# Optimization experiments

Hardware: AMD Instinct MI355X
Metric: run time of the kernel (lower is better)

Reference implementation:

```python
import jax, jax.numpy as jnp
import numpy as np
import math

N = 50000   # nodes
E = 800000  # edges
D = 128     # in/out dim
T = 4       # node types
H = 8       # heads (forced: Linear(8,64).view(-1, H, 8))
DK = D // H
HD = 8      # h_mat feature dim


def setup_inputs() -> dict:
    key = jax.random.key(0)
    ks = jax.random.split(key, 16)
    g = lambda k, shp, fan: jax.random.uniform(k, shp, jnp.float32, -1.0, 1.0) * math.sqrt(6.0 / fan)
    return {
        "meta_xs": jax.random.normal(ks[0], (N, D), jnp.float32),
        "node_type": jax.random.randint(ks[1], (N,), 0, T),
        "edge_index": jax.random.randint(ks[2], (2, E), 0, N),
        "h_mat": jax.random.normal(ks[3], (N, HD), jnp.float32),
        "sub_W": g(ks[4], (T, D, D), 2 * D),
        "sub_b": jnp.zeros((T, D), jnp.float32),
        "neigh_W": g(ks[5], (T, D, D), 2 * D),
        "neigh_b": jnp.zeros((T, D), jnp.float32),
        "hsub_W": g(ks[6], (HD, H * HD), HD + H * HD),
        "hsub_b": jnp.zeros((H * HD,), jnp.float32),
        "hneigh_W": g(ks[7], (HD, H * HD), HD + H * HD),
        "hneigh_b": jnp.zeros((H * HD,), jnp.float32),
        "relation_att": g(ks[8], (T, H, DK), H + DK),
        "relation_h_att": g(ks[9], (T, H, HD), H + HD),
        "ln_gamma": jnp.ones((D,), jnp.float32),
        "ln_beta": jnp.zeros((D,), jnp.float32),
    }


def _hgt_forward(meta_xs, h_mat, sub_W, sub_b, neigh_W, neigh_b, hsub_W, hsub_b,
                 hneigh_W, hneigh_b, relation_att, relation_h_att, ln_gamma, ln_beta,
                 node_type, edge_index):
    n = meta_xs.shape[0]
    e = edge_index.shape[1]
    src = edge_index[0]  # edge_index_j (neighbor)
    dst = edge_index[1]  # edge_index_i (sub / target)
    sqrt_dk = math.sqrt(DK)
    d_h = math.sqrt(H)

    # per-node, type-selected linear projections (sub by own type, neigh by own type)
    q_all = jnp.einsum('nd,tdo->tno', meta_xs, sub_W) + sub_b[:, None, :]      # [T,N,D]
    k_all = jnp.einsum('nd,tdo->tno', meta_xs, neigh_W) + neigh_b[:, None, :]  # [T,N,D]
    ar = jnp.arange(n)
    q_node = q_all[node_type, ar]  # [N,D] sub_linear[type_i](x_i)
    k_node = k_all[node_type, ar]  # [N,D] neigh_linear[type_j](x_j)

    h_sub_node = (h_mat @ hsub_W + hsub_b).reshape(n, H, HD)
    h_neigh_node = (h_mat @ hneigh_W + hneigh_b).reshape(n, H, HD)

    st = node_type[dst]  # sub type per edge selects relation params
    h_s = h_sub_node[dst]    # [E,H,8]
    h_n = h_neigh_node[src]  # [E,H,8]
    att_h = jnp.sum(jnp.tanh(h_s * h_n) * relation_h_att[st], axis=-1) / d_h  # [E,H]

    q_e = q_node[dst].reshape(e, H, DK)
    k_e = k_node[src].reshape(e, H, DK)
    att = jnp.sum(jnp.tanh(q_e * k_e) * relation_att[st], axis=-1) / sqrt_dk * att_h  # [E,H]

    # edge softmax over destination segments
    m = jax.ops.segment_max(att, dst, num_segments=n)  # [N,H]
    ea = jnp.exp(att - m[dst])
    denom = jax.ops.segment_sum(ea, dst, num_segments=n)
    alpha = ea / (denom[dst] + 1e-16)  # [E,H]

    msg = (k_e * alpha[:, :, None]).reshape(e, D)
    aggr = jax.ops.segment_sum(msg, dst, num_segments=n)  # [N,D]

    out = jax.nn.gelu(aggr, approximate=False)
    mu = jnp.mean(out, axis=-1, keepdims=True)
    var = jnp.var(out, axis=-1, keepdims=True)
    return (out - mu) * jax.lax.rsqrt(var + 1e-5) * ln_gamma + ln_beta


def reference(meta_xs, node_type, edge_index, h_mat, sub_W, sub_b, neigh_W, neigh_b,
              hsub_W, hsub_b, hneigh_W, hneigh_b, relation_att, relation_h_att,
              ln_gamma, ln_beta):
    return _hgt_forward(meta_xs, h_mat, sub_W, sub_b, neigh_W, neigh_b, hsub_W, hsub_b,
                        hneigh_W, hneigh_b, relation_att, relation_h_att, ln_gamma, ln_beta,
                        node_type, edge_index)
```

## Files before the change

kernel.cpp:

```cpp
#include <hip/hip_runtime.h>

typedef __bf16 bf16x8 __attribute__((ext_vector_type(8)));
typedef float f32x4 __attribute__((ext_vector_type(4)));

__device__ __forceinline__ float exp2_fast(float x){
#if __has_builtin(__builtin_amdgcn_exp2f)
  return __builtin_amdgcn_exp2f(x);
#else
  return __expf(x * 0.69314718055994531f);
#endif
}
template<int CTRL>
__device__ __forceinline__ float dpp_add(float x){
  union { float f; int i; } a, b;
  a.f = x;
  b.i = __builtin_amdgcn_mov_dpp(a.i, CTRL, 0xF, 0xF, true);
  return x + b.f;
}
__device__ __forceinline__ float sum4(float x){
  x = dpp_add<0xB1>(x);
  x = dpp_add<0x4E>(x);
  return x;
}
__device__ __forceinline__ unsigned int cvt_pk_bf16(float lo, float hi){
  unsigned int r;
  asm("v_cvt_pk_bf16_f32 %0, %1, %2" : "=v"(r) : "v"(lo), "v"(hi));
  return r;
}
__device__ __forceinline__ unsigned short f2bf1(float f){
  return (unsigned short)cvt_pk_bf16(f, f);
}
__device__ __forceinline__ bf16x8 ld_bf8(const unsigned short* p){
  union { uint4 u; bf16x8 v; } c;
  c.u = *reinterpret_cast<const uint4*>(p);
  return c.v;
}
__device__ __forceinline__ bf16x8 ld_f32_to_bf8(const float* p){
  float4 lo = *reinterpret_cast<const float4*>(p);
  float4 hi = *reinterpret_cast<const float4*>(p + 4);
  union { unsigned int u[4]; bf16x8 v; } c;
  c.u[0] = cvt_pk_bf16(lo.x, lo.y);
  c.u[1] = cvt_pk_bf16(lo.z, lo.w);
  c.u[2] = cvt_pk_bf16(hi.x, hi.y);
  c.u[3] = cvt_pk_bf16(hi.z, hi.w);
  return c.v;
}

__global__ void k_ll_h_w(const int* ei, int* cursor, unsigned short* bucket, int E,
                         const int* ntype, int* tcur, int* nbt, int Npad, int N,
                         const float* h_mat, const float* hsW, const float* hsb,
                         const float* hnW, const float* hnb,
                         float2* hs2, char* hnc, int LB, int NB, int HB,
                         const float* subW, const float* neighW,
                         unsigned short* wts, unsigned short* wtn){
  int b = blockIdx.x;
  if (b < LB){
    int i = b*256 + threadIdx.x;
    if (i >= E) return;
    int d = ei[E + i];
    int s = ei[i];
    int pos = atomicAdd(&cursor[d << 4], 1);
    if (pos < 128) bucket[(size_t)d*128 + pos] = (unsigned short)s;
  } else if (b < LB + NB){
    int i = (b - LB)*256 + threadIdx.x;
    if (i >= N) return;
    int lane = threadIdx.x & 63;
    int myt = ntype[i];
    unsigned long long below = (lane == 0) ? 0ull : ((~0ull) >> (64 - lane));
    #pragma unroll
    for (int tt = 0; tt < 4; ++tt){
      unsigned long long mask = __ballot(myt == tt);
      if (mask){
        int leader = __ffsll((long long)mask) - 1;
        int base = 0;
        if (lane == leader) base = atomicAdd(&tcur[tt], __popcll(mask));
        base = __shfl(base, leader);
        if (myt == tt){
          int pos = base + __popcll(mask & below);
          nbt[tt*Npad + pos] = i;
        }
      }
    }
  } else if (b < LB + NB + HB){
    int i = (b - LB - NB)*256 + threadIdx.x;
    if (i >= N*32) return;
    int n = i >> 5, l = i & 31;
    const float* hm = h_mat + (size_t)n*8;
    const float2* hsW2 = reinterpret_cast<const float2*>(hsW);
    const float2* hnW2 = reinterpret_cast<const float2*>(hnW);
    float s0=0.f, s1=0.f, n0=0.f, n1=0.f;
    #pragma unroll
    for (int d = 0; d < 8; ++d){
      float hv = hm[d];
      float2 ws2 = hsW2[d*32 + l];
      float2 wn2 = hnW2[d*32 + l];
      s0 += hv * ws2.x; s1 += hv * ws2.y;
      n0 += hv * wn2.x; n1 += hv * wn2.y;
    }
    float2 bs = reinterpret_cast<const float2*>(hsb)[l];
    float2 bn = reinterpret_cast<const float2*>(hnb)[l];
    hs2[(size_t)i] = make_float2(s0 + bs.x, s1 + bs.y);
    *reinterpret_cast<unsigned int*>(hnc + (size_t)n*128 + l*4)
        = cvt_pk_bf16(n0 + bn.x, n1 + bn.y);
  } else {
    int i = (b - LB - NB - HB)*256 + threadIdx.x;
    int w = i >> 16;
    int r = i & 65535;
    int t = r >> 14;
    int rem = r & 16383;
    int o = rem >> 7;
    int kd = rem & 127;
    const float* src = w ? neighW : subW;
    unsigned short* dstp = w ? wtn : wts;
    dstp[(t << 14) + (o << 7) + kd] = f2bf1(src[(t << 14) + (kd << 7) + o]);
  }
}

__global__ __launch_bounds__(256) void k_qk_mfma(const float* X,
      const unsigned short* wts, const unsigned short* wtn,
      const float* sub_b, const float* neigh_b,
      const int* nbt, const int* tcur, int Npad,
      float* q, char* kkc){
  int b = blockIdx.x;
  int t = -1, chunk = 0, acc = 0;
  #pragma unroll
  for (int tt = 0; tt < 4; ++tt){
    int cnt = tcur[tt];
    int nc = (cnt + 63) >> 6;
    if (t < 0 && b < acc + nc){ t = tt; chunk = b - acc; }
    acc += nc;
  }
  if (t < 0) return;
  int lane = threadIdx.x & 63;
  int w = threadIdx.x >> 6;
  int quad = lane >> 4, l16 = lane & 15;
  int cnt = tcur[t];
  int p = chunk*64 + w*16 + l16;
  bool ok = p < cnt;
  int nid = nbt[t*Npad + (ok ? p : 0)];
  bf16x8 xb[4];
  #pragma unroll
  for (int kk = 0; kk < 4; ++kk)
    xb[kk] = ld_f32_to_bf8(X + (size_t)nid*128 + kk*32 + quad*8);
  #pragma unroll
  for (int pj = 0; pj < 2; ++pj){
    const unsigned short* Wt = pj ? wtn : wts;
    const float* bias = pj ? neigh_b : sub_b;
    #pragma unroll
    for (int ot = 0; ot < 8; ++ot){
      f32x4 c = {0.f, 0.f, 0.f, 0.f};
      #pragma unroll
      for (int kk = 0; kk < 4; ++kk){
        bf16x8 wa = ld_bf8(Wt + ((size_t)t << 14) + ((size_t)(ot*16 + l16) << 7)
                              + kk*32 + quad*8);
        c = __builtin_amdgcn_mfma_f32_16x16x32_bf16(wa, xb[kk], c, 0, 0, 0);
      }
      int o0 = ot*16 + quad*4;
      float4 b4 = *reinterpret_cast<const float4*>(bias + t*128 + o0);
      if (ok){
        if (pj == 0){
          float4 v = make_float4(c[0]+b4.x, c[1]+b4.y, c[2]+b4.z, c[3]+b4.w);
          *reinterpret_cast<float4*>(q + (size_t)nid*128 + o0) = v;
        } else {
          uint2 pk;
          pk.x = cvt_pk_bf16(c[0]+b4.x, c[1]+b4.y);
          pk.y = cvt_pk_bf16(c[2]+b4.z, c[3]+b4.w);
          *reinterpret_cast<uint2*>(kkc + ((size_t)nid << 8) + (size_t)(o0 << 1)) = pk;
        }
      }
    }
  }
}

__global__ __launch_bounds__(256) void k_edge(const float* q, const char* kkc,
      const char* hnc, const float2* hs2, const int* cursor,
      const unsigned short* bucket, const int* ntype,
      const float* rel_att, const float* rel_h_att,
      const float* ln_g, const float* ln_b,
      float* out, int N){
  int wid = (blockIdx.x*blockDim.x + threadIdx.x) >> 6;
  if (wid >= N) return;
  int lane = threadIdx.x & 63;
  int l = lane & 31;
  int half = (lane >> 5) & 1;
  int t4 = l & 3, head = l >> 2;
  const float TLOG2E = 2.8853900817779268f;
  float4 qv = *reinterpret_cast<const float4*>(q + (size_t)wid*128 + l*4);
  float qe0 = qv.x*TLOG2E, qe1 = qv.y*TLOG2E, qe2 = qv.z*TLOG2E, qe3 = qv.w*TLOG2E;
  float2 hv = hs2[(size_t)wid*32 + l];
  float he0 = hv.x*TLOG2E, he1 = hv.y*TLOG2E;
  int st = ntype[wid];
  int rb = st*8 + head;
  float4 ra = *reinterpret_cast<const float4*>(rel_att + rb*16 + t4*4);
  float2 rh = *reinterpret_cast<const float2*>(rel_h_att + rb*8 + t4*2);
  float c0 = -0.5f*ra.x, c1 = -0.5f*ra.y, c2 = -0.5f*ra.z, c3 = -0.5f*ra.w;
  float cs = 0.25f*(ra.x + ra.y + ra.z + ra.w);
  const float HSC = 0.35355339059327373f * 1.4426950408889634f;
  float rh0 = rh.x*HSC, rh1 = rh.y*HSC;
  float ch0 = -2.f*rh0, ch1 = -2.f*rh1, chs = rh0 + rh1;
  float s = 0.f, a0 = 0.f, a1 = 0.f, a2 = 0.f, a3 = 0.f;

  int deg = __builtin_amdgcn_readfirstlane(cursor[wid << 4]);
  if (deg > 128) deg = 128;
  unsigned bkt = reinterpret_cast<const unsigned*>(bucket)[(size_t)wid*64 + lane];
  int niter = (deg + 1) >> 1;
  const char* kk_l = kkc + l*8;
  const char* hn_l = hnc + l*4;

  struct KH { uint2 k; unsigned h; };
  auto lp = [&](int g)->KH {
    int gg = g < niter ? g : 0;
    unsigned v = (unsigned)__builtin_amdgcn_readlane((int)bkt, gg);
    int sA = (int)(v & 0xffffu);
    int sB = (2*gg + 1 < deg) ? (int)(v >> 16) : sA;
    int sy = half ? sB : sA;
    KH r;
    r.k = *reinterpret_cast<const uint2*>(kk_l + ((size_t)(unsigned)sy << 8));
    r.h = *reinterpret_cast<const unsigned*>(hn_l + ((size_t)(unsigned)sy << 7));
    return r;
  };
  auto pr = [&](KH P, int g){
    union { unsigned u; float f; } k0,k1,k2,k3,h0,h1;
    k0.u = P.k.x << 16; k1.u = P.k.x & 0xffff0000u;
    k2.u = P.k.y << 16; k3.u = P.k.y & 0xffff0000u;
    h0.u = P.h << 16;   h1.u = P.h & 0xffff0000u;
    float e0 = exp2_fast(qe0*k0.f), e1 = exp2_fast(qe1*k1.f);
    float e2 = exp2_fast(qe2*k2.f), e3 = exp2_fast(qe3*k3.f);
    float f0 = exp2_fast(he0*h0.f), f1 = exp2_fast(he1*h1.f);
    float r0 = __builtin_amdgcn_rcpf(e0 + 1.f), r1 = __builtin_amdgcn_rcpf(e1 + 1.f);
    float r2 = __builtin_amdgcn_rcpf(e2 + 1.f), r3 = __builtin_amdgcn_rcpf(e3 + 1.f);
    float g0 = __builtin_amdgcn_rcpf(f0 + 1.f), g1 = __builtin_amdgcn_rcpf(f1 + 1.f);
    float pp = fmaf(c0,r0, fmaf(c1,r1, fmaf(c2,r2, fmaf(c3,r3, cs))));
    float ph = fmaf(ch0,g0, fmaf(ch1,g1, chs));
    pp = sum4(pp);
    ph = sum4(ph);
    float w = exp2_fast(pp * ph);
    w = (2*g + half < deg) ? w : 0.f;
    s += w;
    a0 = fmaf(w, k0.f, a0); a1 = fmaf(w, k1.f, a1);
    a2 = fmaf(w, k2.f, a2); a3 = fmaf(w, k3.f, a3);
  };

  if (niter > 0){
    KH A = lp(0);
    KH B = lp(1);
    for (int g = 0; g < niter; g += 2){
      KH C = lp(g+2);
      pr(A, g);
      KH D = lp(g+3);
      if (g+1 < niter) pr(B, g+1);
      A = C; B = D;
    }
  }
  s  += __shfl_xor(s, 32);
  a0 += __shfl_xor(a0, 32); a1 += __shfl_xor(a1, 32);
  a2 += __shfl_xor(a2, 32); a3 += __shfl_xor(a3, 32);

  float inv = 1.0f / (s + 1e-16f);
  float x0 = a0*inv, x1 = a1*inv, x2 = a2*inv, x3 = a3*inv;
  const float IS2 = 0.70710678118654752f;
  x0 = 0.5f*x0*(1.f + erff(x0*IS2));
  x1 = 0.5f*x1*(1.f + erff(x1*IS2));
  x2 = 0.5f*x2*(1.f + erff(x2*IS2));
  x3 = 0.5f*x3*(1.f + erff(x3*IS2));
  float sm = x0+x1+x2+x3;
  float sq = x0*x0 + x1*x1 + x2*x2 + x3*x3;
  #pragma unroll
  for (int d = 1; d < 32; d <<= 1){ sm += __shfl_xor(sm, d); sq += __shfl_xor(sq, d); }
  float mu = sm * (1.f/128.f);
  float var = fmaxf(sq * (1.f/128.f) - mu*mu, 0.f);
  float r = rsqrtf(var + 1e-5f);
  if (half == 0){
    float4 g4 = *reinterpret_cast<const float4*>(ln_g + l*4);
    float4 b4 = *reinterpret_cast<const float4*>(ln_b + l*4);
    float4 o4 = make_float4((x0-mu)*r*g4.x + b4.x, (x1-mu)*r*g4.y + b4.y,
                            (x2-mu)*r*g4.z + b4.z, (x3-mu)*r*g4.w + b4.w);
    *reinterpret_cast<float4*>(out + (size_t)wid*128 + l*4) = o4;
  }
}

extern "C" void kernel_launch(void* const* d_in, const int* in_sizes, int n_in,
                              void* d_out, int out_size, void* d_ws, size_t ws_size,
                              hipStream_t stream) {
  const float* meta_xs  = (const float*)d_in[0];
  const int*   node_type= (const int*)d_in[1];
  const int*   edge_idx = (const int*)d_in[2];
  const float* h_mat    = (const float*)d_in[3];
  const float* sub_W    = (const float*)d_in[4];
  const float* sub_b    = (const float*)d_in[5];
  const float* neigh_W  = (const float*)d_in[6];
  const float* neigh_b  = (const float*)d_in[7];
  const float* hsub_W   = (const float*)d_in[8];
  const float* hsub_b   = (const float*)d_in[9];
  const float* hneigh_W = (const float*)d_in[10];
  const float* hneigh_b = (const float*)d_in[11];
  const float* rel_att  = (const float*)d_in[12];
  const float* rel_hatt = (const float*)d_in[13];
  const float* ln_g     = (const float*)d_in[14];
  const float* ln_b     = (const float*)d_in[15];

  const int N = in_sizes[0] / 128;
  const int E = in_sizes[2] / 2;
  const int Npad = (N + 63) & ~63;

  char* wbase = (char*)d_ws;
  size_t o = 0;
  auto carve = [&](size_t bytes)->char* {
    char* p = wbase + o;
    o = (o + bytes + 255) & ~(size_t)255;
    return p;
  };
  float*          q      = (float*)carve((size_t)N*128*4);
  char*           kkc    = carve((size_t)N*256);
  char*           hnc    = carve((size_t)N*128);
  float2*         hs2    = (float2*)carve((size_t)N*32*8);
  unsigned short* bucket = (unsigned short*)carve((size_t)N*128*2);
  int*            cursor = (int*)carve((size_t)N*16*4);
  int*            tmeta  = (int*)carve(64);
  int*            nbt    = (int*)carve((size_t)4*Npad*4);
  unsigned short* wts    = (unsigned short*)carve((size_t)4*128*128*2);
  unsigned short* wtn    = (unsigned short*)carve((size_t)4*128*128*2);
  if (o > ws_size) return;

  int* tcur = tmeta;

  const int LB = (E + 255) / 256;
  const int NB = (N + 255) / 256;
  const int HB = (N*32 + 255) / 256;
  const int WB = (2*4*128*128) / 256;

  hipMemsetAsync(cursor, 0, (size_t)N*64 + 64, stream);
  k_ll_h_w  <<<LB + NB + HB + WB, 256, 0, stream>>>(edge_idx, cursor, bucket, E,
                                               node_type, tcur, nbt, Npad, N,
                                               h_mat, hsub_W, hsub_b, hneigh_W, hneigh_b,
                                               hs2, hnc, LB, NB, HB,
                                               sub_W, neigh_W, wts, wtn);
  k_qk_mfma <<<((N+63)>>6)+4, 256, 0, stream>>>(meta_xs, wts, wtn, sub_b, neigh_b,
                                                nbt, tcur, Npad, q, kkc);
  k_edge    <<<(N+3)/4, 256, 0, stream>>>(q, kkc, hnc, hs2, cursor, bucket, node_type,
                                          rel_att, rel_hatt, ln_g, ln_b,
                                          (float*)d_out, N);
}
```

Measured before the change: 290.4 us.

## Co-schedule edge bucketing and h-projection with MFMA QK projection kernel

Regroups work across the prep kernels. The first kernel now only does type-sorting of nodes and weight transpose. The edge bucketing (atomics) and h_mat projections move into the same launch as the MFMA Q/K projection, so the latency-bound atomic scatter overlaps with compute. Edge bucketing also becomes a grid-stride loop with 512 blocks that issues four independent atomics per thread to raise memory-level parallelism. The risk is contention and imbalance between block roles in the mixed kernel.

```diff
diff --git a/kernel.cpp b/kernel.cpp
--- a/kernel.cpp
+++ b/kernel.cpp
@@ -46,23 +46,12 @@
   return c.v;
 }
 
-__global__ void k_ll_h_w(const int* ei, int* cursor, unsigned short* bucket, int E,
-                         const int* ntype, int* tcur, int* nbt, int Npad, int N,
-                         const float* h_mat, const float* hsW, const float* hsb,
-                         const float* hnW, const float* hnb,
-                         float2* hs2, char* hnc, int LB, int NB, int HB,
-                         const float* subW, const float* neighW,
-                         unsigned short* wts, unsigned short* wtn){
+__global__ void k_prep(const int* ntype, int* tcur, int* nbt, int Npad, int N,
+                       const float* subW, const float* neighW,
+                       unsigned short* wts, unsigned short* wtn, int NB){
   int b = blockIdx.x;
-  if (b < LB){
+  if (b < NB){
     int i = b*256 + threadIdx.x;
-    if (i >= E) return;
-    int d = ei[E + i];
-    int s = ei[i];
-    int pos = atomicAdd(&cursor[d << 4], 1);
-    if (pos < 128) bucket[(size_t)d*128 + pos] = (unsigned short)s;
-  } else if (b < LB + NB){
-    int i = (b - LB)*256 + threadIdx.x;
     if (i >= N) return;
     int lane = threadIdx.x & 63;
     int myt = ntype[i];
@@ -81,29 +70,8 @@
         }
       }
     }
-  } else if (b < LB + NB + HB){
-    int i = (b - LB - NB)*256 + threadIdx.x;
-    if (i >= N*32) return;
-    int n = i >> 5, l = i & 31;
-    const float* hm = h_mat + (size_t)n*8;
-    const float2* hsW2 = reinterpret_cast<const float2*>(hsW);
-    const float2* hnW2 = reinterpret_cast<const float2*>(hnW);
-    float s0=0.f, s1=0.f, n0=0.f, n1=0.f;
-    #pragma unroll
-    for (int d = 0; d < 8; ++d){
-      float hv = hm[d];
-      float2 ws2 = hsW2[d*32 + l];
-      float2 wn2 = hnW2[d*32 + l];
-      s0 += hv * ws2.x; s1 += hv * ws2.y;
-      n0 += hv * wn2.x; n1 += hv * wn2.y;
-    }
-    float2 bs = reinterpret_cast<const float2*>(hsb)[l];
-    float2 bn = reinterpret_cast<const float2*>(hnb)[l];
-    hs2[(size_t)i] = make_float2(s0 + bs.x, s1 + bs.y);
-    *reinterpret_cast<unsigned int*>(hnc + (size_t)n*128 + l*4)
-        = cvt_pk_bf16(n0 + bn.x, n1 + bn.y);
   } else {
-    int i = (b - LB - NB - HB)*256 + threadIdx.x;
+    int i = (b - NB)*256 + threadIdx.x;
     int w = i >> 16;
     int r = i & 65535;
     int t = r >> 14;
@@ -116,59 +84,108 @@
   }
 }
 
-__global__ __launch_bounds__(256) void k_qk_mfma(const float* X,
+__global__ __launch_bounds__(256) void k_mix(const float* X,
       const unsigned short* wts, const unsigned short* wtn,
       const float* sub_b, const float* neigh_b,
       const int* nbt, const int* tcur, int Npad,
-      float* q, char* kkc){
+      float* q, char* kkc,
+      const int* ei, int* cursor, unsigned short* bucket, int E,
+      const float* h_mat, const float* hsW, const float* hsb,
+      const float* hnW, const float* hnb,
+      float2* hs2, char* hnc, int N, int MB, int SB){
   int b = blockIdx.x;
-  int t = -1, chunk = 0, acc = 0;
-  #pragma unroll
-  for (int tt = 0; tt < 4; ++tt){
-    int cnt = tcur[tt];
-    int nc = (cnt + 63) >> 6;
-    if (t < 0 && b < acc + nc){ t = tt; chunk = b - acc; }
-    acc += nc;
-  }
-  if (t < 0) return;
-  int lane = threadIdx.x & 63;
-  int w = threadIdx.x >> 6;
-  int quad = lane >> 4, l16 = lane & 15;
-  int cnt = tcur[t];
-  int p = chunk*64 + w*16 + l16;
-  bool ok = p < cnt;
-  int nid = nbt[t*Npad + (ok ? p : 0)];
-  bf16x8 xb[4];
-  #pragma unroll
-  for (int kk = 0; kk < 4; ++kk)
-    xb[kk] = ld_f32_to_bf8(X + (size_t)nid*128 + kk*32 + quad*8);
-  #pragma unroll
-  for (int pj = 0; pj < 2; ++pj){
-    const unsigned short* Wt = pj ? wtn : wts;
-    const float* bias = pj ? neigh_b : sub_b;
-    #pragma unroll
-    for (int ot = 0; ot < 8; ++ot){
-      f32x4 c = {0.f, 0.f, 0.f, 0.f};
+  if (b < MB){
+    int t = -1, chunk = 0, acc = 0;
+    #pragma unroll
+    for (int tt = 0; tt < 4; ++tt){
+      int cnt = tcur[tt];
+      int nc = (cnt + 63) >> 6;
+      if (t < 0 && b < acc + nc){ t = tt; chunk = b - acc; }
+      acc += nc;
+    }
+    if (t < 0) return;
+    int lane = threadIdx.x & 63;
+    int w = threadIdx.x >> 6;
+    int quad = lane >> 4, l16 = lane & 15;
+    int cnt = tcur[t];
+    int p = chunk*64 + w*16 + l16;
+    bool ok = p < cnt;
+    int nid = nbt[t*Npad + (ok ? p : 0)];
+    bf16x8 xb[4];
+    #pragma unroll
+    for (int kk = 0; kk < 4; ++kk)
+      xb[kk] = ld_f32_to_bf8(X + (size_t)nid*128 + kk*32 + quad*8);
+    #pragma unroll
+    for (int pj = 0; pj < 2; ++pj){
+      const unsigned short* Wt = pj ? wtn : wts;
+      const float* bias = pj ? neigh_b : sub_b;
       #pragma unroll
-      for (int kk = 0; kk < 4; ++kk){
-        bf16x8 wa = ld_bf8(Wt + ((size_t)t << 14) + ((size_t)(ot*16 + l16) << 7)
-                              + kk*32 + quad*8);
-        c = __builtin_amdgcn_mfma_f32_16x16x32_bf16(wa, xb[kk], c, 0, 0, 0);
-      }
-      int o0 = ot*16 + quad*4;
-      float4 b4 = *reinterpret_cast<const float4*>(bias + t*128 + o0);
-      if (ok){
-        if (pj == 0){
-          float4 v = make_float4(c[0]+b4.x, c[1]+b4.y, c[2]+b4.z, c[3]+b4.w);
-          *reinterpret_cast<float4*>(q + (size_t)nid*128 + o0) = v;
-        } else {
-          uint2 pk;
-          pk.x = cvt_pk_bf16(c[0]+b4.x, c[1]+b4.y);
-          pk.y = cvt_pk_bf16(c[2]+b4.z, c[3]+b4.w);
-          *reinterpret_cast<uint2*>(kkc + ((size_t)nid << 8) + (size_t)(o0 << 1)) = pk;
+      for (int ot = 0; ot < 8; ++ot){
+        f32x4 c = {0.f, 0.f, 0.f, 0.f};
+        #pragma unroll
+        for (int kk = 0; kk < 4; ++kk){
+          bf16x8 wa = ld_bf8(Wt + ((size_t)t << 14) + ((size_t)(ot*16 + l16) << 7)
+                                + kk*32 + quad*8);
+          c = __builtin_amdgcn_mfma_f32_16x16x32_bf16(wa, xb[kk], c, 0, 0, 0);
+        }
+        int o0 = ot*16 + quad*4;
+        float4 b4 = *reinterpret_cast<const float4*>(bias + t*128 + o0);
+        if (ok){
+          if (pj == 0){
+            float4 v = make_float4(c[0]+b4.x, c[1]+b4.y, c[2]+b4.z, c[3]+b4.w);
+            *reinterpret_cast<float4*>(q + (size_t)nid*128 + o0) = v;
+          } else {
+            uint2 pk;
+            pk.x = cvt_pk_bf16(c[0]+b4.x, c[1]+b4.y);
+            pk.y = cvt_pk_bf16(c[2]+b4.z, c[3]+b4.w);
+            *reinterpret_cast<uint2*>(kkc + ((size_t)nid << 8) + (size_t)(o0 << 1)) = pk;
+          }
         }
       }
     }
+  } else if (b < MB + SB){
+    int tid = (b - MB)*256 + threadIdx.x;
+    const int stride = SB*256;
+    for (int base = tid; base < E; base += 4*stride){
+      int i0 = base;
+      int i1 = base + stride;
+      int i2 = base + 2*stride;
+      int i3 = base + 3*stride;
+      int d0 = ei[E+i0], s0 = ei[i0];
+      int d1 = -1, s1 = 0, d2 = -1, s2 = 0, d3 = -1, s3 = 0;
+      if (i1 < E){ d1 = ei[E+i1]; s1 = ei[i1]; }
+      if (i2 < E){ d2 = ei[E+i2]; s2 = ei[i2]; }
+      if (i3 < E){ d3 = ei[E+i3]; s3 = ei[i3]; }
+      int p0 = atomicAdd(&cursor[d0 << 4], 1);
+      int p1 = (d1 >= 0) ? atomicAdd(&cursor[d1 << 4], 1) : 128;
+      int p2 = (d2 >= 0) ? atomicAdd(&cursor[d2 << 4], 1) : 128;
+      int p3 = (d3 >= 0) ? atomicAdd(&cursor[d3 << 4], 1) : 128;
+      if (p0 < 128) bucket[(size_t)d0*128 + p0] = (unsigned short)s0;
+      if (p1 < 128) bucket[(size_t)d1*128 + p1] = (unsigned short)s1;
+      if (p2 < 128) bucket[(size_t)d2*128 + p2] = (unsigned short)s2;
+      if (p3 < 128) bucket[(size_t)d3*128 + p3] = (unsigned short)s3;
+    }
+  } else {
+    int i = (b - MB - SB)*256 + threadIdx.x;
+    if (i >= N*32) return;
+    int n = i >> 5, l = i & 31;
+    const float* hm = h_mat + (size_t)n*8;
+    const float2* hsW2 = reinterpret_cast<const float2*>(hsW);
+    const float2* hnW2 = reinterpret_cast<const float2*>(hnW);
+    float s0=0.f, s1=0.f, n0=0.f, n1=0.f;
+    #pragma unroll
+    for (int d = 0; d < 8; ++d){
+      float hv = hm[d];
+      float2 ws2 = hsW2[d*32 + l];
+      float2 wn2 = hnW2[d*32 + l];
+      s0 += hv * ws2.x; s1 += hv * ws2.y;
+      n0 += hv * wn2.x; n1 += hv * wn2.y;
+    }
+    float2 bs = reinterpret_cast<const float2*>(hsb)[l];
+    float2 bn = reinterpret_cast<const float2*>(hnb)[l];
+    hs2[(size_t)i] = make_float2(s0 + bs.x, s1 + bs.y);
+    *reinterpret_cast<unsigned int*>(hnc + (size_t)n*128 + l*4)
+        = cvt_pk_bf16(n0 + bn.x, n1 + bn.y);
   }
 }
 
@@ -324,20 +341,21 @@
 
   int* tcur = tmeta;
 
-  const int LB = (E + 255) / 256;
   const int NB = (N + 255) / 256;
+  const int WB = (2*4*128*128) / 256;
+  const int MB = ((N + 63) >> 6) + 4;
+  const int SB = 512;
   const int HB = (N*32 + 255) / 256;
-  const int WB = (2*4*128*128) / 256;
 
   hipMemsetAsync(cursor, 0, (size_t)N*64 + 64, stream);
-  k_ll_h_w  <<<LB + NB + HB + WB, 256, 0, stream>>>(edge_idx, cursor, bucket, E,
-                                               node_type, tcur, nbt, Npad, N,
-                                               h_mat, hsub_W, hsub_b, hneigh_W, hneigh_b,
-                                               hs2, hnc, LB, NB, HB,
-                                               sub_W, neigh_W, wts, wtn);
-  k_qk_mfma <<<((N+63)>>6)+4, 256, 0, stream>>>(meta_xs, wts, wtn, sub_b, neigh_b,
-                                                nbt, tcur, Npad, q, kkc);
-  k_edge    <<<(N+3)/4, 256, 0, stream>>>(q, kkc, hnc, hs2, cursor, bucket, node_type,
-                                          rel_att, rel_hatt, ln_g, ln_b,
-                                          (float*)d_out, N);
-}
+  k_prep <<<NB + WB, 256, 0, stream>>>(node_type, tcur, nbt, Npad, N,
+                                       sub_W, neigh_W, wts, wtn, NB);
+  k_mix  <<<MB + SB + HB, 256, 0, stream>>>(meta_xs, wts, wtn, sub_b, neigh_b,
+                                       nbt, tcur, Npad, q, kkc,
+                                       edge_idx, cursor, bucket, E,
+                                       h_mat, hsub_W, hsub_b, hneigh_W, hneigh_b,
+                                       hs2, hnc, N, MB, SB);
+  k_edge <<<(N+3)/4, 256, 0, stream>>>(q, kkc, hnc, hs2, cursor, bucket, node_type,
+                                       rel_att, rel_hatt, ln_g, ln_b,
+                                       (float*)d_out, N);
+}
```

After: 285.0 us. Within noise of the previous version (-1.8%).

## Replace global-atomic edge bucketing with LDS histogram, scan, and scatter passes

Applied to the files above, without the earlier changes.

Builds the per-destination edge buckets in three steps. Per-chunk LDS histograms of destination counts (packed 16-bit pairs) are computed over node ranges, a per-node prefix scan over chunks follows, then a second pass scatters source ids using LDS atomics seeded with the scanned offsets. This removes the contended global atomics on a padded cursor array and the large memset. The scatter and h-projection work is fused into the MFMA projection launch. The cost is reading edge_index twice per range and an extra launch for the scan.

```diff
diff --git a/kernel.cpp b/kernel.cpp
--- a/kernel.cpp
+++ b/kernel.cpp
@@ -2,6 +2,9 @@
 
 typedef __bf16 bf16x8 __attribute__((ext_vector_type(8)));
 typedef float f32x4 __attribute__((ext_vector_type(4)));
+
+#define B_CHUNK 64
+#define R_RANGE 4
 
 __device__ __forceinline__ float exp2_fast(float x){
 #if __has_builtin(__builtin_amdgcn_exp2f)
@@ -46,23 +49,16 @@
   return c.v;
 }
 
-__global__ void k_ll_h_w(const int* ei, int* cursor, unsigned short* bucket, int E,
-                         const int* ntype, int* tcur, int* nbt, int Npad, int N,
-                         const float* h_mat, const float* hsW, const float* hsb,
-                         const float* hnW, const float* hnb,
-                         float2* hs2, char* hnc, int LB, int NB, int HB,
-                         const float* subW, const float* neighW,
-                         unsigned short* wts, unsigned short* wtn){
+__global__ __launch_bounds__(256) void k_prep(const int* ntype, int* tcur, int* nbt,
+                       int Npad, int N,
+                       const float* subW, const float* neighW,
+                       unsigned short* wts, unsigned short* wtn,
+                       const int* ei, int E, unsigned short* hist,
+                       int RNG, int HR, int NB, int WB){
+  __shared__ unsigned int lsh[6272];
   int b = blockIdx.x;
-  if (b < LB){
+  if (b < NB){
     int i = b*256 + threadIdx.x;
-    if (i >= E) return;
-    int d = ei[E + i];
-    int s = ei[i];
-    int pos = atomicAdd(&cursor[d << 4], 1);
-    if (pos < 128) bucket[(size_t)d*128 + pos] = (unsigned short)s;
-  } else if (b < LB + NB){
-    int i = (b - LB)*256 + threadIdx.x;
     if (i >= N) return;
     int lane = threadIdx.x & 63;
     int myt = ntype[i];
@@ -81,8 +77,140 @@
         }
       }
     }
-  } else if (b < LB + NB + HB){
-    int i = (b - LB - NB)*256 + threadIdx.x;
+  } else if (b < NB + WB){
+    int i = (b - NB)*256 + threadIdx.x;
+    int w = i >> 16;
+    int r = i & 65535;
+    int t = r >> 14;
+    int rem = r & 16383;
+    int o = rem >> 7;
+    int kd = rem & 127;
+    const float* src = w ? neighW : subW;
+    unsigned short* dstp = w ? wtn : wts;
+    dstp[(t << 14) + (o << 7) + kd] = f2bf1(src[(t << 14) + (kd << 7) + o]);
+  } else {
+    int sb = b - NB - WB;
+    int cb = sb & (B_CHUNK - 1);
+    int r  = sb / B_CHUNK;
+    int lo = r * RNG;
+    int half = RNG >> 1;
+    for (int i = threadIdx.x; i < half; i += 256) lsh[i] = 0;
+    __syncthreads();
+    int C = (E + B_CHUNK - 1) / B_CHUNK;
+    int e0 = cb * C;
+    int e1 = e0 + C; if (e1 > E) e1 = E;
+    for (int i = e0 + threadIdx.x; i < e1; i += 256){
+      int d = ei[E + i] - lo;
+      if ((unsigned)d < (unsigned)RNG)
+        atomicAdd(&lsh[d >> 1], (d & 1) ? 65536u : 1u);
+    }
+    __syncthreads();
+    unsigned int* hrow = reinterpret_cast<unsigned int*>(hist + (size_t)cb*HR + lo);
+    for (int i = threadIdx.x; i < half; i += 256) hrow[i] = lsh[i];
+  }
+}
+
+__global__ __launch_bounds__(256) void k_scan(unsigned short* hist, int HR,
+                                              int* deg, int N){
+  int d = blockIdx.x*256 + threadIdx.x;
+  if (d >= N) return;
+  unsigned run = 0;
+  #pragma unroll 4
+  for (int b = 0; b < B_CHUNK; ++b){
+    unsigned short* p = hist + (size_t)b*HR + d;
+    unsigned v = *p;
+    *p = (unsigned short)run;
+    run += v;
+  }
+  deg[d] = (int)run;
+}
+
+__global__ __launch_bounds__(256) void k_mix(const float* X,
+      const unsigned short* wts, const unsigned short* wtn,
+      const float* sub_b, const float* neigh_b,
+      const int* nbt, const int* tcur, int Npad,
+      float* q, char* kkc,
+      const int* ei, unsigned short* bucket, int E,
+      unsigned short* hist, int RNG, int HR,
+      const float* h_mat, const float* hsW, const float* hsb,
+      const float* hnW, const float* hnb,
+      float2* hs2, char* hnc, int N, int MB, int SBL){
+  __shared__ unsigned int lsh[6272];
+  int b = blockIdx.x;
+  if (b < MB){
+    int t = -1, chunk = 0, acc = 0;
+    #pragma unroll
+    for (int tt = 0; tt < 4; ++tt){
+      int cnt = tcur[tt];
+      int nc = (cnt + 63) >> 6;
+      if (t < 0 && b < acc + nc){ t = tt; chunk = b - acc; }
+      acc += nc;
+    }
+    if (t < 0) return;
+    int lane = threadIdx.x & 63;
+    int w = threadIdx.x >> 6;
+    int quad = lane >> 4, l16 = lane & 15;
+    int cnt = tcur[t];
+    int p = chunk*64 + w*16 + l16;
+    bool ok = p < cnt;
+    int nid = nbt[t*Npad + (ok ? p : 0)];
+    bf16x8 xb[4];
+    #pragma unroll
+    for (int kk = 0; kk < 4; ++kk)
+      xb[kk] = ld_f32_to_bf8(X + (size_t)nid*128 + kk*32 + quad*8);
+    #pragma unroll
+    for (int pj = 0; pj < 2; ++pj){
+      const unsigned short* Wt = pj ? wtn : wts;
+      const float* bias = pj ? neigh_b : sub_b;
+      #pragma unroll
+      for (int ot = 0; ot < 8; ++ot){
+        f32x4 c = {0.f, 0.f, 0.f, 0.f};
+        #pragma unroll
+        for (int kk = 0; kk < 4; ++kk){
+          bf16x8 wa = ld_bf8(Wt + ((size_t)t << 14) + ((size_t)(ot*16 + l16) << 7)
+                                + kk*32 + quad*8);
+          c = __builtin_amdgcn_mfma_f32_16x16x32_bf16(wa, xb[kk], c, 0, 0, 0);
+        }
+        int o0 = ot*16 + quad*4;
+        float4 b4 = *reinterpret_cast<const float4*>(bias + t*128 + o0);
+        if (ok){
+          if (pj == 0){
+            float4 v = make_float4(c[0]+b4.x, c[1]+b4.y, c[2]+b4.z, c[3]+b4.w);
+            *reinterpret_cast<float4*>(q + (size_t)nid*128 + o0) = v;
+          } else {
+            uint2 pk;
+            pk.x = cvt_pk_bf16(c[0]+b4.x, c[1]+b4.y);
+            pk.y = cvt_pk_bf16(c[2]+b4.z, c[3]+b4.w);
+            *reinterpret_cast<uint2*>(kkc + ((size_t)nid << 8) + (size_t)(o0 << 1)) = pk;
+          }
+        }
+      }
+    }
+  } else if (b < MB + SBL){
+    int sb = b - MB;
+    int cb = sb & (B_CHUNK - 1);
+    int r  = sb / B_CHUNK;
+    int lo = r * RNG;
+    int half = RNG >> 1;
+    const unsigned int* hrow =
+        reinterpret_cast<const unsigned int*>(hist + (size_t)cb*HR + lo);
+    for (int i = threadIdx.x; i < half; i += 256) lsh[i] = hrow[i];
+    __syncthreads();
+    int C = (E + B_CHUNK - 1) / B_CHUNK;
+    int e0 = cb * C;
+    int e1 = e0 + C; if (e1 > E) e1 = E;
+    for (int i = e0 + threadIdx.x; i < e1; i += 256){
+      int d = ei[E + i];
+      int rb = d - lo;
+      if ((unsigned)rb < (unsigned)RNG){
+        unsigned old = atomicAdd(&lsh[rb >> 1], (rb & 1) ? 65536u : 1u);
+        unsigned pos = (old >> ((rb & 1) << 4)) & 0xffffu;
+        if (pos < 128)
+          bucket[(size_t)d*128 + pos] = (unsigned short)ei[i];
+      }
+    }
+  } else {
+    int i = (b - MB - SBL)*256 + threadIdx.x;
     if (i >= N*32) return;
     int n = i >> 5, l = i & 31;
     const float* hm = h_mat + (size_t)n*8;
@@ -102,78 +230,11 @@
     hs2[(size_t)i] = make_float2(s0 + bs.x, s1 + bs.y);
     *reinterpret_cast<unsigned int*>(hnc + (size_t)n*128 + l*4)
         = cvt_pk_bf16(n0 + bn.x, n1 + bn.y);
-  } else {
-    int i = (b - LB - NB - HB)*256 + threadIdx.x;
-    int w = i >> 16;
-    int r = i & 65535;
-    int t = r >> 14;
-    int rem = r & 16383;
-    int o = rem >> 7;
-    int kd = rem & 127;
-    const float* src = w ? neighW : subW;
-    unsigned short* dstp = w ? wtn : wts;
-    dstp[(t << 14) + (o << 7) + kd] = f2bf1(src[(t << 14) + (kd << 7) + o]);
   }
 }
 
-__global__ __launch_bounds__(256) void k_qk_mfma(const float* X,
-      const unsigned short* wts, const unsigned short* wtn,
-      const float* sub_b, const float* neigh_b,
-      const int* nbt, const int* tcur, int Npad,
-      float* q, char* kkc){
-  int b = blockIdx.x;
-  int t = -1, chunk = 0, acc = 0;
-  #pragma unroll
-  for (int tt = 0; tt < 4; ++tt){
-    int cnt = tcur[tt];
-    int nc = (cnt + 63) >> 6;
-    if (t < 0 && b < acc + nc){ t = tt; chunk = b - acc; }
-    acc += nc;
-  }
-  if (t < 0) return;
-  int lane = threadIdx.x & 63;
-  int w = threadIdx.x >> 6;
-  int quad = lane >> 4, l16 = lane & 15;
-  int cnt = tcur[t];
-  int p = chunk*64 + w*16 + l16;
-  bool ok = p < cnt;
-  int nid = nbt[t*Npad + (ok ? p : 0)];
-  bf16x8 xb[4];
-  #pragma unroll
-  for (int kk = 0; kk < 4; ++kk)
-    xb[kk] = ld_f32_to_bf8(X + (size_t)nid*128 + kk*32 + quad*8);
-  #pragma unroll
-  for (int pj = 0; pj < 2; ++pj){
-    const unsigned short* Wt = pj ? wtn : wts;
-    const float* bias = pj ? neigh_b : sub_b;
-    #pragma unroll
-    for (int ot = 0; ot < 8; ++ot){
-      f32x4 c = {0.f, 0.f, 0.f, 0.f};
-      #pragma unroll
-      for (int kk = 0; kk < 4; ++kk){
-        bf16x8 wa = ld_bf8(Wt + ((size_t)t << 14) + ((size_t)(ot*16 + l16) << 7)
-                              + kk*32 + quad*8);
-        c = __builtin_amdgcn_mfma_f32_16x16x32_bf16(wa, xb[kk], c, 0, 0, 0);
-      }
-      int o0 = ot*16 + quad*4;
-      float4 b4 = *reinterpret_cast<const float4*>(bias + t*128 + o0);
-      if (ok){
-        if (pj == 0){
-          float4 v = make_float4(c[0]+b4.x, c[1]+b4.y, c[2]+b4.z, c[3]+b4.w);
-          *reinterpret_cast<float4*>(q + (size_t)nid*128 + o0) = v;
-        } else {
-          uint2 pk;
-          pk.x = cvt_pk_bf16(c[0]+b4.x, c[1]+b4.y);
-          pk.y = cvt_pk_bf16(c[2]+b4.z, c[3]+b4.w);
-          *reinterpret_cast<uint2*>(kkc + ((size_t)nid << 8) + (size_t)(o0 << 1)) = pk;
-        }
-      }
-    }
-  }
-}
-
 __global__ __launch_bounds__(256) void k_edge(const float* q, const char* kkc,
-      const char* hnc, const float2* hs2, const int* cursor,
+      const char* hnc, const float2* hs2, const int* degA,
       const unsigned short* bucket, const int* ntype,
       const float* rel_att, const float* rel_h_att,
       const float* ln_g, const float* ln_b,
@@ -200,7 +261,7 @@
   float ch0 = -2.f*rh0, ch1 = -2.f*rh1, chs = rh0 + rh1;
   float s = 0.f, a0 = 0.f, a1 = 0.f, a2 = 0.f, a3 = 0.f;
 
-  int deg = __builtin_amdgcn_readfirstlane(cursor[wid << 4]);
+  int deg = __builtin_amdgcn_readfirstlane(degA[wid]);
   if (deg > 128) deg = 128;
   unsigned bkt = reinterpret_cast<const unsigned*>(bucket)[(size_t)wid*64 + lane];
   int niter = (deg + 1) >> 1;
@@ -302,6 +363,8 @@
   const int N = in_sizes[0] / 128;
   const int E = in_sizes[2] / 2;
   const int Npad = (N + 63) & ~63;
+  const int RNG = (((N + R_RANGE - 1) / R_RANGE) + 1) & ~1;
+  const int HR  = RNG * R_RANGE;
 
   char* wbase = (char*)d_ws;
   size_t o = 0;
@@ -315,7 +378,8 @@
   char*           hnc    = carve((size_t)N*128);
   float2*         hs2    = (float2*)carve((size_t)N*32*8);
   unsigned short* bucket = (unsigned short*)carve((size_t)N*128*2);
-  int*            cursor = (int*)carve((size_t)N*16*4);
+  unsigned short* hist   = (unsigned short*)carve((size_t)B_CHUNK*HR*2);
+  int*            deg    = (int*)carve((size_t)N*4);
   int*            tmeta  = (int*)carve(64);
   int*            nbt    = (int*)carve((size_t)4*Npad*4);
   unsigned short* wts    = (unsigned short*)carve((size_t)4*128*128*2);
@@ -324,20 +388,23 @@
 
   int* tcur = tmeta;
 
-  const int LB = (E + 255) / 256;
-  const int NB = (N + 255) / 256;
-  const int HB = (N*32 + 255) / 256;
-  const int WB = (2*4*128*128) / 256;
-
-  hipMemsetAsync(cursor, 0, (size_t)N*64 + 64, stream);
-  k_ll_h_w  <<<LB + NB + HB + WB, 256, 0, stream>>>(edge_idx, cursor, bucket, E,
-                                               node_type, tcur, nbt, Npad, N,
-                                               h_mat, hsub_W, hsub_b, hneigh_W, hneigh_b,
-                                               hs2, hnc, LB, NB, HB,
-                                               sub_W, neigh_W, wts, wtn);
-  k_qk_mfma <<<((N+63)>>6)+4, 256, 0, stream>>>(meta_xs, wts, wtn, sub_b, neigh_b,
-                                                nbt, tcur, Npad, q, kkc);
-  k_edge    <<<(N+3)/4, 256, 0, stream>>>(q, kkc, hnc, hs2, cursor, bucket, node_type,
-                                          rel_att, rel_hatt, ln_g, ln_b,
-                                          (float*)d_out, N);
-}
+  const int NB  = (N + 255) / 256;
+  const int WB  = (2*4*128*128) / 256;
+  const int SBL = B_CHUNK * R_RANGE;
+  const int MB  = ((N + 63) >> 6) + 4;
+  const int HB  = (N*32 + 255) / 256;
+
+  hipMemsetAsync(tmeta, 0, 64, stream);
+  k_prep <<<NB + WB + SBL, 256, 0, stream>>>(node_type, tcur, nbt, Npad, N,
+                                       sub_W, neigh_W, wts, wtn,
+                                       edge_idx, E, hist, RNG, HR, NB, WB);
+  k_scan <<<(N + 255)/256, 256, 0, stream>>>(hist, HR, deg, N);
+  k_mix  <<<MB + SBL + HB, 256, 0, stream>>>(meta_xs, wts, wtn, sub_b, neigh_b,
+                                       nbt, tcur, Npad, q, kkc,
+                                       edge_idx, bucket, E, hist, RNG, HR,
+                                       h_mat, hsub_W, hsub_b, hneigh_W, hneigh_b,
+                                       hs2, hnc, N, MB, SBL);
+  k_edge <<<(N+3)/4, 256, 0, stream>>>(q, kkc, hnc, hs2, deg, bucket, node_type,
+                                       rel_att, rel_hatt, ln_g, ln_b,
+                                       (float*)d_out, N);
+}
```

Measured after the change: 292.5 us. No clear change (+0.7%).
